# Kernel optimization log

Measured on AMD Instinct MI355X. Metric: run time of the kernel, lower is better.

The kernel has to match this reference:

```python
import jax, jax.numpy as jnp
import numpy as np

NUM_HEADS = 16
WINDOW = 128  # local-attention half-width used by the mask generator
NEG_INF = -1e9


def setup_inputs() -> dict:
    key = jax.random.key(0)
    ks = jax.random.split(key, 12)
    T, N, C = 2048, 2, 1024
    s = 1.0 / np.sqrt(C)
    inp = {
        "q": jax.random.normal(ks[0], (T, N, C), jnp.float32),
        "k": jax.random.normal(ks[1], (T, N, C), jnp.float32),
        "v": jax.random.normal(ks[2], (T, N, C), jnp.float32),
        # MultiHeadDispatch: separate q/k/v input projections + output projection (with bias)
        "Wq": jax.random.normal(ks[3], (C, C), jnp.float32) * s,
        "bq": jnp.zeros((C,), jnp.float32),
        "Wk": jax.random.normal(ks[4], (C, C), jnp.float32) * s,
        "bk": jnp.zeros((C,), jnp.float32),
        "Wv": jax.random.normal(ks[5], (C, C), jnp.float32) * s,
        "bv": jnp.zeros((C,), jnp.float32),
        "Wo": jax.random.normal(ks[6], (C, C), jnp.float32) * s,
        "bo": jnp.zeros((C,), jnp.float32),
        "key_length": jax.random.randint(ks[7], (N,), 1, T, dtype=jnp.int32),
    }
    return inp


def _build_mask(Lq, Lk, key_length):
    # mask_generator: banded local-window mask, True = attend
    i = jnp.arange(Lq)[:, None]
    j = jnp.arange(Lk)[None, :]
    local = jnp.abs(i - j) <= WINDOW                      # (Lq, Lk)
    # forward(): mask[i, :, :key_length[i]] = 1  -> unmask prefix keys per batch elem
    prefix = j[None, :, :] < key_length[:, None, None]    # (N, Lq, Lk)
    return local[None, :, :] | prefix                     # (N, Lq, Lk) bool


def reference(q, k, v, Wq, bq, Wk, bk, Wv, bv, Wo, bo, key_length):
    T, N, C = q.shape
    H = NUM_HEADS
    Dh = C // H
    mask = _build_mask(q.shape[0], k.shape[0], key_length)  # (N, Lq, Lk)

    def heads(x, W, b):
        # (T, N, C) -> project -> (N, H, T, Dh)
        y = x @ W.T + b
        return jnp.transpose(y.reshape(x.shape[0], N, H, Dh), (1, 2, 0, 3))

    qh = heads(q, Wq, bq)
    kh = heads(k, Wk, bk)
    vh = heads(v, Wv, bv)

    scale = 1.0 / np.sqrt(Dh).astype(np.float32)
    scores = jnp.einsum('nhqd,nhkd->nhqk', qh, kh) * scale  # (N, H, Lq, Lk)
    scores = jnp.where(mask[:, None, :, :], scores, NEG_INF)
    att = jax.nn.softmax(scores, axis=-1)
    y = jnp.einsum('nhqk,nhkd->nhqd', att, vh)              # (N, H, Lq, Dh)
    y = jnp.transpose(y, (2, 0, 1, 3)).reshape(T, N, C)     # back to (t, n, c)
    return y @ Wo.T + bo
```

## Files before the change

### kernel.cpp

```cpp
#include <hip/hip_runtime.h>
#include <math.h>

#define T_DIM 2048
#define N_B   2
#define C_DIM 1024
#define H_DIM 16
#define DH    64
#define M_DIM 4096
#define WIN   128

typedef _Float16 h8 __attribute__((ext_vector_type(8)));
typedef float    f4 __attribute__((ext_vector_type(4)));

#if __has_builtin(__builtin_amdgcn_exp2f)
#define EXP2(x) __builtin_amdgcn_exp2f(x)
#else
#define EXP2(x) __expf((x) * 0.693147180559945f)
#endif

__device__ __forceinline__ void glds16(const _Float16* g, _Float16* l) {
    typedef const __attribute__((address_space(1))) unsigned int guint;
    typedef __attribute__((address_space(3))) unsigned int luint;
    __builtin_amdgcn_global_load_lds((guint*)g, (luint*)l, 16, 0, 0);
}

struct CvtA { const float* s; _Float16* d; int n; };
struct Cvt7 { CvtA a[7]; };

__global__ __launch_bounds__(256) void cvt_k(Cvt7 c) {
    CvtA A = c.a[blockIdx.y];
    const int i = (blockIdx.x * 256 + threadIdx.x) * 8;
    if (i >= A.n) return;
    const float4 v0 = *(const float4*)&A.s[i];
    const float4 v1 = *(const float4*)&A.s[i + 4];
    h8 o;
    o[0] = (_Float16)v0.x; o[1] = (_Float16)v0.y;
    o[2] = (_Float16)v0.z; o[3] = (_Float16)v0.w;
    o[4] = (_Float16)v1.x; o[5] = (_Float16)v1.y;
    o[6] = (_Float16)v1.z; o[7] = (_Float16)v1.w;
    *(h8*)&A.d[i] = o;
}

struct QkvArgs {
    const _Float16* x[3];
    const _Float16* w[3];
    const float*    b[3];
    _Float16*       out[3];
};

__global__ __launch_bounds__(256) void proj_qkv(QkvArgs args) {
    const int z = blockIdx.z;
    const _Float16* __restrict__ A = args.x[z];
    const _Float16* __restrict__ B = args.w[z];
    const float* __restrict__ bias = args.b[z];
    _Float16* __restrict__ out     = args.out[z];

    __shared__ _Float16 Asm[2][128 * 32];
    __shared__ _Float16 Bsm[2][128 * 32];
    const int tid  = threadIdx.x;
    const int lane = tid & 63;
    const int wave = tid >> 6;
    const int wr = wave >> 1, wc = wave & 1;
    const int l15 = lane & 15, hi = lane >> 4;
    const int m0 = blockIdx.x << 7;
    const int o0 = blockIdx.y << 7;

    auto STAGE = [&](int b, int k0) {
#pragma unroll
        for (int c = 0; c < 2; ++c) {
            const int chunk = tid + c * 256;
            const int row = chunk >> 2, c4 = chunk & 3;
            const int sc = (c4 ^ ((row >> 1) & 3)) << 3;
            glds16(&A[(size_t)(m0 + row) * C_DIM + k0 + sc], &Asm[b][chunk << 3]);
            glds16(&B[(size_t)(o0 + row) * C_DIM + k0 + sc], &Bsm[b][chunk << 3]);
        }
    };

    f4 acc[4][4];
    const f4 z4 = {0.f, 0.f, 0.f, 0.f};
#pragma unroll
    for (int i = 0; i < 4; ++i)
#pragma unroll
        for (int j = 0; j < 4; ++j) acc[i][j] = z4;

    STAGE(0, 0);
    __syncthreads();
    int buf = 0;
    for (int k0 = 0; k0 < C_DIM; k0 += 32) {
        if (k0 + 32 < C_DIM) STAGE(buf ^ 1, k0 + 32);

        h8 a[4], b[4];
#pragma unroll
        for (int mr = 0; mr < 4; ++mr) {
            const int R = wr * 64 + mr * 16 + l15;
            a[mr] = *(const h8*)&Asm[buf][R * 32 + ((hi ^ ((R >> 1) & 3)) << 3)];
        }
#pragma unroll
        for (int nf = 0; nf < 4; ++nf) {
            const int R = wc * 64 + nf * 16 + l15;
            b[nf] = *(const h8*)&Bsm[buf][R * 32 + ((hi ^ ((R >> 1) & 3)) << 3)];
        }
#pragma unroll
        for (int mr = 0; mr < 4; ++mr)
#pragma unroll
            for (int nf = 0; nf < 4; ++nf)
                acc[mr][nf] = __builtin_amdgcn_mfma_f32_16x16x32_f16(
                    a[mr], b[nf], acc[mr][nf], 0, 0, 0);

        __syncthreads();
        buf ^= 1;
    }

#pragma unroll
    for (int nf = 0; nf < 4; ++nf) {
        const int o = o0 + wc * 64 + nf * 16 + l15;
        const float bb = bias[o];
        const int hh = o >> 6, d = o & 63;
#pragma unroll
        for (int mr = 0; mr < 4; ++mr)
#pragma unroll
            for (int reg = 0; reg < 4; ++reg) {
                const int m = m0 + wr * 64 + mr * 16 + 4 * hi + reg;
                const float val = acc[mr][nf][reg] + bb;
                const int t = m >> 1, n = m & 1;
                if (z == 2) {
                    out[(((size_t)(n * H_DIM + hh)) * DH + d) * T_DIM + t] = (_Float16)val;
                } else {
                    out[(((size_t)(n * H_DIM + hh)) * T_DIM + t) * DH + d] = (_Float16)val;
                }
            }
    }
}

__global__ __launch_bounds__(256) void proj_o(
    const _Float16* __restrict__ A, const _Float16* __restrict__ B,
    const float* __restrict__ bias, float* __restrict__ out)
{
    __shared__ _Float16 Asm[2][128 * 32];
    __shared__ _Float16 Bsm[2][128 * 32];
    const int tid  = threadIdx.x;
    const int lane = tid & 63;
    const int wave = tid >> 6;
    const int wr = wave >> 1, wc = wave & 1;
    const int l15 = lane & 15, hi = lane >> 4;
    const int m0 = blockIdx.x << 7;
    const int o0 = blockIdx.y << 7;

    auto STAGE = [&](int b, int k0) {
#pragma unroll
        for (int c = 0; c < 2; ++c) {
            const int chunk = tid + c * 256;
            const int row = chunk >> 2, c4 = chunk & 3;
            const int sc = (c4 ^ ((row >> 1) & 3)) << 3;
            glds16(&A[(size_t)(m0 + row) * C_DIM + k0 + sc], &Asm[b][chunk << 3]);
            glds16(&B[(size_t)(o0 + row) * C_DIM + k0 + sc], &Bsm[b][chunk << 3]);
        }
    };

    f4 acc[4][4];
    const f4 z4 = {0.f, 0.f, 0.f, 0.f};
#pragma unroll
    for (int i = 0; i < 4; ++i)
#pragma unroll
        for (int j = 0; j < 4; ++j) acc[i][j] = z4;

    STAGE(0, 0);
    __syncthreads();
    int buf = 0;
    for (int k0 = 0; k0 < C_DIM; k0 += 32) {
        if (k0 + 32 < C_DIM) STAGE(buf ^ 1, k0 + 32);

        h8 a[4], b[4];
#pragma unroll
        for (int mr = 0; mr < 4; ++mr) {
            const int R = wr * 64 + mr * 16 + l15;
            a[mr] = *(const h8*)&Asm[buf][R * 32 + ((hi ^ ((R >> 1) & 3)) << 3)];
        }
#pragma unroll
        for (int nf = 0; nf < 4; ++nf) {
            const int R = wc * 64 + nf * 16 + l15;
            b[nf] = *(const h8*)&Bsm[buf][R * 32 + ((hi ^ ((R >> 1) & 3)) << 3)];
        }
#pragma unroll
        for (int mr = 0; mr < 4; ++mr)
#pragma unroll
            for (int nf = 0; nf < 4; ++nf)
                acc[mr][nf] = __builtin_amdgcn_mfma_f32_16x16x32_f16(
                    a[mr], b[nf], acc[mr][nf], 0, 0, 0);

        __syncthreads();
        buf ^= 1;
    }

#pragma unroll
    for (int nf = 0; nf < 4; ++nf) {
        const int o = o0 + wc * 64 + nf * 16 + l15;
        const float bb = bias[o];
#pragma unroll
        for (int mr = 0; mr < 4; ++mr)
#pragma unroll
            for (int reg = 0; reg < 4; ++reg) {
                const int m = m0 + wr * 64 + mr * 16 + 4 * hi + reg;
                out[(size_t)m * C_DIM + o] = acc[mr][nf][reg] + bb;
            }
    }
}

__global__ __launch_bounds__(256, 2) void attn_v7(
    const _Float16* __restrict__ QH, const _Float16* __restrict__ KH,
    const _Float16* __restrict__ VT, const int* __restrict__ key_length,
    _Float16* __restrict__ Y)
{
    __shared__ _Float16 Ks[2][64 * 64];
    __shared__ _Float16 Vs[2][64 * 64];
    __shared__ _Float16 Ps[4][32 * 72];

    const int nh = blockIdx.x;
    const int n  = nh >> 4;
    const int h  = nh & 15;
    const int qb = blockIdx.y << 7;
    const int kl = key_length[n];
    const int tid  = threadIdx.x;
    const int wave = tid >> 6;
    const int lane = tid & 63;
    const int l15 = lane & 15, hi = lane >> 4;
    const int qw = qb + wave * 32;
    const int swz = l15 & 7;

    const size_t hb = (size_t)nh * T_DIM * DH;
    const _Float16* Qb = QH + hb;
    const _Float16* Kb = KH + hb;
    const _Float16* Vb = VT + hb;

    const int klc0 = ((kl + 63) >> 6) << 6;
    const int klc  = (klc0 < T_DIM) ? klc0 : T_DIM;
    const int blo  = (qb >= WIN) ? ((qb - WIN) & ~63) : 0;
    int bhi = ((qb + 127 + WIN) >> 6) << 6;
    if (bhi > T_DIM - 64) bhi = T_DIM - 64;
    auto nxt = [&](int k0) -> int {
        k0 += 64;
        if (k0 < klc) return k0;
        if (k0 < blo) k0 = blo;
        return (k0 <= bhi) ? k0 : -1;
    };

    auto STAGE = [&](int b, int k0) {
#pragma unroll
        for (int c = 0; c < 2; ++c) {
            const int slot = wave * 128 + c * 64 + lane;
            const int r = slot >> 3, c16 = slot & 7;
            const int sc = (c16 ^ (r & 7)) << 3;
            glds16(&Kb[(size_t)(k0 + r) * DH + sc], &Ks[b][slot << 3]);
        }
#pragma unroll
        for (int c = 0; c < 2; ++c) {
            const int slot = wave * 128 + c * 64 + lane;
            const int r = slot >> 3, c16 = slot & 7;
            const int sc = (c16 ^ (r & 7)) << 3;
            glds16(&Vb[(size_t)r * T_DIM + k0 + sc], &Vs[b][slot << 3]);
        }
    };

    h8 qa[2][2];
#pragma unroll
    for (int mr = 0; mr < 2; ++mr)
#pragma unroll
        for (int ks = 0; ks < 2; ++ks)
            qa[mr][ks] = *(const h8*)&Qb[(size_t)(qw + mr * 16 + l15) * DH + ks * 32 + hi * 8];

    f4 O[2][4];
    const f4 z4 = {0.f, 0.f, 0.f, 0.f};
#pragma unroll
    for (int mr = 0; mr < 2; ++mr)
#pragma unroll
        for (int df = 0; df < 4; ++df) O[mr][df] = z4;
    float m_i[2][4], lp[2][4];
#pragma unroll
    for (int mr = 0; mr < 2; ++mr)
#pragma unroll
        for (int r = 0; r < 4; ++r) { m_i[mr][r] = -1e30f; lp[mr][r] = 0.f; }

    const float SC = 0.18033688f;

    auto TILE = [&](int b, int k0) {
        h8 kb[2][4];
#pragma unroll
        for (int ks = 0; ks < 2; ++ks)
#pragma unroll
            for (int cf = 0; cf < 4; ++cf)
                kb[ks][cf] = *(const h8*)&Ks[b][(cf * 16 + l15) * 64 +
                                                (((ks * 4 + hi) ^ swz) << 3)];

        f4 sacc[2][4];
#pragma unroll
        for (int mr = 0; mr < 2; ++mr)
#pragma unroll
            for (int cf = 0; cf < 4; ++cf) sacc[mr][cf] = z4;
#pragma unroll
        for (int ks = 0; ks < 2; ++ks)
#pragma unroll
            for (int mr = 0; mr < 2; ++mr)
#pragma unroll
                for (int cf = 0; cf < 4; ++cf)
                    sacc[mr][cf] = __builtin_amdgcn_mfma_f32_16x16x32_f16(
                        qa[mr][ks], kb[ks][cf], sacc[mr][cf], 0, 0, 0);

        h8 vb[2][4];
#pragma unroll
        for (int ks = 0; ks < 2; ++ks)
#pragma unroll
            for (int df = 0; df < 4; ++df)
                vb[ks][df] = *(const h8*)&Vs[b][(df * 16 + l15) * 64 +
                                                (((ks * 4 + hi) ^ swz) << 3)];

        const bool full = (k0 + 63 < kl) ||
                          (k0 >= qw + 31 - WIN && k0 + 63 <= qw + WIN);

#pragma unroll
        for (int mr = 0; mr < 2; ++mr) {
            if (full) {
#pragma unroll
                for (int cf = 0; cf < 4; ++cf)
#pragma unroll
                    for (int reg = 0; reg < 4; ++reg)
                        sacc[mr][cf][reg] *= SC;
            } else {
#pragma unroll
                for (int cf = 0; cf < 4; ++cf)
#pragma unroll
                    for (int reg = 0; reg < 4; ++reg) {
                        const int i = qw + mr * 16 + 4 * hi + reg;
                        const int j = k0 + cf * 16 + l15;
                        const int dd = i - j;
                        const bool ok = (dd <= WIN && dd >= -WIN) || (j < kl);
                        sacc[mr][cf][reg] = ok ? sacc[mr][cf][reg] * SC : -1e9f;
                    }
            }
        }

        float lm[2][4];
        bool need = false;
#pragma unroll
        for (int mr = 0; mr < 2; ++mr)
#pragma unroll
            for (int reg = 0; reg < 4; ++reg) {
                lm[mr][reg] = fmaxf(fmaxf(sacc[mr][0][reg], sacc[mr][1][reg]),
                                    fmaxf(sacc[mr][2][reg], sacc[mr][3][reg]));
                need = need || (lm[mr][reg] > m_i[mr][reg]);
            }
        if (__any(need)) {
#pragma unroll
            for (int mr = 0; mr < 2; ++mr)
#pragma unroll
                for (int reg = 0; reg < 4; ++reg) {
                    float mt = lm[mr][reg];
                    mt = fmaxf(mt, __shfl_xor(mt, 1));
                    mt = fmaxf(mt, __shfl_xor(mt, 2));
                    mt = fmaxf(mt, __shfl_xor(mt, 4));
                    mt = fmaxf(mt, __shfl_xor(mt, 8));
                    const float mnew = fmaxf(m_i[mr][reg], mt + 3.0f);
                    const float rr = EXP2(m_i[mr][reg] - mnew);
                    m_i[mr][reg] = mnew;
                    lp[mr][reg] *= rr;
#pragma unroll
                    for (int df = 0; df < 4; ++df) O[mr][df][reg] *= rr;
                }
        }

        _Float16* Pw = &Ps[wave][0];
#pragma unroll
        for (int mr = 0; mr < 2; ++mr)
#pragma unroll
            for (int reg = 0; reg < 4; ++reg) {
                const int row = mr * 16 + 4 * hi + reg;
                const float mi = m_i[mr][reg];
                float acc = 0.f;
#pragma unroll
                for (int cf = 0; cf < 4; ++cf) {
                    const float p = EXP2(sacc[mr][cf][reg] - mi);
                    acc += p;
                    Pw[row * 72 + cf * 16 + l15] = (_Float16)p;
                }
                lp[mr][reg] += acc;
            }

        h8 pa[2][2];
#pragma unroll
        for (int mr = 0; mr < 2; ++mr)
#pragma unroll
            for (int ks = 0; ks < 2; ++ks)
                pa[mr][ks] = *(const h8*)&Pw[(mr * 16 + l15) * 72 + ks * 32 + hi * 8];
#pragma unroll
        for (int ks = 0; ks < 2; ++ks)
#pragma unroll
            for (int mr = 0; mr < 2; ++mr)
#pragma unroll
                for (int df = 0; df < 4; ++df)
                    O[mr][df] = __builtin_amdgcn_mfma_f32_16x16x32_f16(
                        pa[mr][ks], vb[ks][df], O[mr][df], 0, 0, 0);
    };

    STAGE(0, 0);
    __syncthreads();
    int buf = 0, k0 = 0, k1 = nxt(0);
    for (;;) {
        if (k1 >= 0) STAGE(buf ^ 1, k1);
        const bool wkeep = (k0 < kl) || (k0 <= qw + 31 + WIN && k0 + 63 >= qw - WIN);
        if (wkeep) TILE(buf, k0);
        __syncthreads();
        if (k1 < 0) break;
        k0 = k1; k1 = nxt(k0); buf ^= 1;
    }

    float lf[2][4];
#pragma unroll
    for (int mr = 0; mr < 2; ++mr)
#pragma unroll
        for (int reg = 0; reg < 4; ++reg) {
            float l = lp[mr][reg];
            l += __shfl_xor(l, 1); l += __shfl_xor(l, 2);
            l += __shfl_xor(l, 4); l += __shfl_xor(l, 8);
            lf[mr][reg] = l;
        }

#pragma unroll
    for (int mr = 0; mr < 2; ++mr)
#pragma unroll
        for (int reg = 0; reg < 4; ++reg) {
            const float inv = 1.f / lf[mr][reg];
            const int i = qw + mr * 16 + 4 * hi + reg;
#pragma unroll
            for (int df = 0; df < 4; ++df) {
                Y[((size_t)i * N_B + n) * C_DIM + h * DH + df * 16 + l15] =
                    (_Float16)(O[mr][df][reg] * inv);
            }
        }
}

extern "C" void kernel_launch(void* const* d_in, const int* in_sizes, int n_in,
                              void* d_out, int out_size, void* d_ws, size_t ws_size,
                              hipStream_t stream) {
    const float* q  = (const float*)d_in[0];
    const float* k  = (const float*)d_in[1];
    const float* v  = (const float*)d_in[2];
    const float* Wq = (const float*)d_in[3];
    const float* bq = (const float*)d_in[4];
    const float* Wk = (const float*)d_in[5];
    const float* bk = (const float*)d_in[6];
    const float* Wv = (const float*)d_in[7];
    const float* bv = (const float*)d_in[8];
    const float* Wo = (const float*)d_in[9];
    const float* bo = (const float*)d_in[10];
    const int*   kl = (const int*)d_in[11];

    const int NX = M_DIM * C_DIM;
    const int NW = C_DIM * C_DIM;

    _Float16* xq = (_Float16*)d_ws;
    _Float16* xk = xq + NX;
    _Float16* xv = xk + NX;
    _Float16* wq = xv + NX;
    _Float16* wk = wq + NW;
    _Float16* wv = wk + NW;
    _Float16* wo = wv + NW;
    _Float16* QHh = wo + NW;
    _Float16* KHh = QHh + NX;
    _Float16* VTh = KHh + NX;
    _Float16* Yh  = xq;

    Cvt7 c;
    c.a[0] = {q,  xq, NX}; c.a[1] = {k,  xk, NX}; c.a[2] = {v,  xv, NX};
    c.a[3] = {Wq, wq, NW}; c.a[4] = {Wk, wk, NW};
    c.a[5] = {Wv, wv, NW}; c.a[6] = {Wo, wo, NW};
    cvt_k<<<dim3(NX / (256 * 8), 7), 256, 0, stream>>>(c);

    QkvArgs qa;
    qa.x[0] = xq; qa.x[1] = xk; qa.x[2] = xv;
    qa.w[0] = wq; qa.w[1] = wk; qa.w[2] = wv;
    qa.b[0] = bq; qa.b[1] = bk; qa.b[2] = bv;
    qa.out[0] = QHh; qa.out[1] = KHh; qa.out[2] = VTh;
    proj_qkv<<<dim3(M_DIM / 128, C_DIM / 128, 3), 256, 0, stream>>>(qa);

    attn_v7<<<dim3(N_B * H_DIM, T_DIM / 128), 256, 0, stream>>>(QHh, KHh, VTh, kl, Yh);

    proj_o<<<dim3(M_DIM / 128, C_DIM / 128), 256, 0, stream>>>(Yh, wo, bo, (float*)d_out);
}
```

Before: 111.3 us.

## Triple-buffer projection GEMM LDS staging with one barrier per k-step

Both projection GEMM kernels move from double to triple-buffered LDS, with two k-tiles prefetched ahead. A manual vmcnt wait plus a single s_barrier per iteration replaces the two __syncthreads. The goal is to hide global-to-LDS load latency behind the MFMA work and cut barrier overhead. In exchange LDS use per block rises to 48KB, which may reduce occupancy, and correctness depends on the hand-counted vmcnt matching the four outstanding loads per stage.

```diff
diff --git a/kernel.cpp b/kernel.cpp
--- a/kernel.cpp
+++ b/kernel.cpp
@@ -55,8 +55,8 @@
     const float* __restrict__ bias = args.b[z];
     _Float16* __restrict__ out     = args.out[z];
 
-    __shared__ _Float16 Asm[2][128 * 32];
-    __shared__ _Float16 Bsm[2][128 * 32];
+    __shared__ _Float16 Asm[3][128 * 32];
+    __shared__ _Float16 Bsm[3][128 * 32];
     const int tid  = threadIdx.x;
     const int lane = tid & 63;
     const int wave = tid >> 6;
@@ -84,10 +84,20 @@
         for (int j = 0; j < 4; ++j) acc[i][j] = z4;
 
     STAGE(0, 0);
-    __syncthreads();
+    STAGE(1, 32);
     int buf = 0;
     for (int k0 = 0; k0 < C_DIM; k0 += 32) {
-        if (k0 + 32 < C_DIM) STAGE(buf ^ 1, k0 + 32);
+        if (k0 + 32 < C_DIM) {
+            asm volatile("s_waitcnt vmcnt(4)" ::: "memory");
+        } else {
+            asm volatile("s_waitcnt vmcnt(0)" ::: "memory");
+        }
+        __builtin_amdgcn_s_barrier();
+        __builtin_amdgcn_sched_barrier(0);
+        if (k0 + 64 < C_DIM) {
+            const int nb = (buf + 2 >= 3) ? buf - 1 : buf + 2;
+            STAGE(nb, k0 + 64);
+        }
 
         h8 a[4], b[4];
 #pragma unroll
@@ -107,8 +117,7 @@
                 acc[mr][nf] = __builtin_amdgcn_mfma_f32_16x16x32_f16(
                     a[mr], b[nf], acc[mr][nf], 0, 0, 0);
 
-        __syncthreads();
-        buf ^= 1;
+        buf = (buf + 1 >= 3) ? 0 : buf + 1;
     }
 
 #pragma unroll
@@ -136,8 +145,8 @@
     const _Float16* __restrict__ A, const _Float16* __restrict__ B,
     const float* __restrict__ bias, float* __restrict__ out)
 {
-    __shared__ _Float16 Asm[2][128 * 32];
-    __shared__ _Float16 Bsm[2][128 * 32];
+    __shared__ _Float16 Asm[3][128 * 32];
+    __shared__ _Float16 Bsm[3][128 * 32];
     const int tid  = threadIdx.x;
     const int lane = tid & 63;
     const int wave = tid >> 6;
@@ -165,10 +174,20 @@
         for (int j = 0; j < 4; ++j) acc[i][j] = z4;
 
     STAGE(0, 0);
-    __syncthreads();
+    STAGE(1, 32);
     int buf = 0;
     for (int k0 = 0; k0 < C_DIM; k0 += 32) {
-        if (k0 + 32 < C_DIM) STAGE(buf ^ 1, k0 + 32);
+        if (k0 + 32 < C_DIM) {
+            asm volatile("s_waitcnt vmcnt(4)" ::: "memory");
+        } else {
+            asm volatile("s_waitcnt vmcnt(0)" ::: "memory");
+        }
+        __builtin_amdgcn_s_barrier();
+        __builtin_amdgcn_sched_barrier(0);
+        if (k0 + 64 < C_DIM) {
+            const int nb = (buf + 2 >= 3) ? buf - 1 : buf + 2;
+            STAGE(nb, k0 + 64);
+        }
 
         h8 a[4], b[4];
 #pragma unroll
@@ -188,8 +207,7 @@
                 acc[mr][nf] = __builtin_amdgcn_mfma_f32_16x16x32_f16(
                     a[mr], b[nf], acc[mr][nf], 0, 0, 0);
 
-        __syncthreads();
-        buf ^= 1;
+        buf = (buf + 1 >= 3) ? 0 : buf + 1;
     }
 
 #pragma unroll
```

New measurement: 113.3 us. Within noise of the previous version (+1.8%).
